# Performance work log

Hardware: AMD Instinct MI355X
Metric: run time of the kernel (lower is better)

## Reference

```python
import jax, jax.numpy as jnp
import numpy as np


def setup_inputs() -> dict:
    key = jax.random.key(0)
    ks = jax.random.split(key, 12)
    B, N, Din, D, K = 2, 1024, 64, 64, 24
    s = lambda fan_in: 1.0 / np.sqrt(fan_in)
    return {
        "feature": jax.random.normal(ks[0], (B, N, Din), jnp.float32),
        "xyz": jax.random.normal(ks[1], (B, N, 3), jnp.float32),
        "pw1": jax.random.uniform(ks[2], (Din, D), jnp.float32, -s(Din), s(Din)),
        "pb1": jax.random.uniform(ks[3], (D,), jnp.float32, -s(Din), s(Din)),
        "pw2": jax.random.uniform(ks[4], (D, D), jnp.float32, -s(D), s(D)),
        "pb2": jax.random.uniform(ks[5], (D,), jnp.float32, -s(D), s(D)),
        "rw": jax.random.uniform(ks[6], (3, D * D), jnp.float32, -s(3), s(3)),
        "rb": jax.random.uniform(ks[7], (D * D,), jnp.float32, -s(3), s(3)),
        "sw": jax.random.uniform(ks[8], (D, D), jnp.float32, -s(D), s(D)),
        "sb": jax.random.uniform(ks[9], (D,), jnp.float32, -s(D), s(D)),
        "knn_num": 24,
    }


def reference(feature, xyz, pw1, pb1, pw2, pb2, rw, rb, sw, sb, knn_num):
    B, N, _ = feature.shape
    D = pw2.shape[1]
    K = knn_num
    # KNN over xyz (squared euclidean distances, smallest K)
    sq = jnp.sum(xyz * xyz, axis=-1)  # [B,N]
    d2 = sq[:, :, None] + sq[:, None, :] - 2.0 * jnp.einsum('bnc,bmc->bnm', xyz, xyz)
    _, idx = jax.lax.top_k(-d2, K)  # [B,N,K]
    bidx = jnp.arange(B)[:, None, None]
    rel = xyz[bidx, idx] - xyz[:, :, None, :]  # [B,N,K,3]
    # prefix MLP: relu(Linear -> ReLU -> Linear)
    feat = jax.nn.relu(jax.nn.relu(feature @ pw1 + pb1) @ pw2 + pb2)  # [B,N,D]
    # per-edge weight generation + softmax over (K*D)
    w = (rel @ rw + rb).reshape(B, N, K * D, D)
    w = jax.nn.softmax(w, axis=-2)
    # gather neighbor features and aggregate
    gv = feat[bidx, idx].reshape(B, N, K * D)  # [B,N,K*D]
    out = jnp.einsum('bnm,bnmd->bnd', gv, w)  # [B,N,D]
    out = out @ sw + sb
    return (out, N)
```

## Files before the change

### kernel.cpp

```cpp
#include <hip/hip_runtime.h>
#include <math.h>

#define BB 2
#define NN 1024
#define DD 64
#define KK 24
#define NPTS (BB * NN)

#if __has_builtin(__builtin_amdgcn_exp2f)
#define EXP2(x) __builtin_amdgcn_exp2f(x)
#else
#define EXP2(x) exp2f(x)
#endif


__global__ __launch_bounds__(256) void prep_kernel(const float* __restrict__ rw,
                                                   const float* __restrict__ rb,
                                                   float* __restrict__ rwS,
                                                   float* __restrict__ rbS) {
    const float LOG2E = 1.4426950408889634f;
    int i = blockIdx.x * 256 + threadIdx.x;
    if (i < 3 * 4096) {
        rwS[i] = rw[i] * LOG2E;
    } else {
        int j = i - 3 * 4096;
        if (j < 4096) rbS[j] = rb[j] * LOG2E;
    }
}

__global__ __launch_bounds__(256) void mlp_kernel(const float* __restrict__ feature,
                                                  const float* __restrict__ pw1,
                                                  const float* __restrict__ pb1,
                                                  const float* __restrict__ pw2,
                                                  const float* __restrict__ pb2,
                                                  float* __restrict__ feat) {
    int tid = threadIdx.x;
    int r = tid >> 6;
    int d = tid & 63;
    int row = blockIdx.x * 4 + r;
    __shared__ float s_in[4][64];
    __shared__ float s_h[4][64];
    s_in[r][d] = feature[row * 64 + d];
    __syncthreads();
    float h = pb1[d];
#pragma unroll
    for (int i = 0; i < 64; i++) h = __builtin_fmaf(s_in[r][i], pw1[i * 64 + d], h);
    h = fmaxf(h, 0.f);
    s_h[r][d] = h;
    __syncthreads();
    float f = pb2[d];
#pragma unroll
    for (int i = 0; i < 64; i++) f = __builtin_fmaf(s_h[r][i], pw2[i * 64 + d], f);
    f = fmaxf(f, 0.f);
    feat[row * 64 + d] = f;
}

__global__ __launch_bounds__(64) void knn_kernel(const float* __restrict__ xyz,
                                                 int* __restrict__ idx_out) {
    int pt = blockIdx.x;
    int b = pt >> 10;
    int n = pt & 1023;
    int lane = threadIdx.x;
    const float* xb = xyz + (size_t)b * NN * 3;
    float xn = xb[n * 3 + 0], yn = xb[n * 3 + 1], zn = xb[n * 3 + 2];
    float sqn = xn * xn + yn * yn + zn * zn;
    float dist[16];
#pragma unroll
    for (int c = 0; c < 16; c++) {
        int m = c * 64 + lane;
        float xm = xb[m * 3 + 0], ym = xb[m * 3 + 1], zm = xb[m * 3 + 2];
        float sqm = xm * xm + ym * ym + zm * zm;
        float dot = xn * xm + yn * ym + zn * zm;
        dist[c] = sqn + sqm - 2.0f * dot;
    }
    for (int r = 0; r < KK; r++) {
        float best = 3.4e38f;
        int bi = 1 << 30;
#pragma unroll
        for (int c = 0; c < 16; c++) {
            if (dist[c] < best) {
                best = dist[c];
                bi = c * 64 + lane;
            }
        }
#pragma unroll
        for (int off = 32; off >= 1; off >>= 1) {
            float ob = __shfl_down(best, off);
            int oi = __shfl_down(bi, off);
            if (ob < best || (ob == best && oi < bi)) {
                best = ob;
                bi = oi;
            }
        }
        bi = __shfl(bi, 0);
        if ((bi & 63) == lane) dist[bi >> 6] = 3.4e38f;
        if (lane == 0) idx_out[pt * KK + r] = bi;
    }
}

__global__ __launch_bounds__(256) void agg_kernel(const float* __restrict__ xyz,
                                                  const float* __restrict__ feat,
                                                  const int* __restrict__ idx,
                                                  const float* __restrict__ rwS,
                                                  const float* __restrict__ rbS,
                                                  const float* __restrict__ sw,
                                                  const float* __restrict__ sb,
                                                  float* __restrict__ out) {
    int pt = blockIdx.x;
    int b = pt >> 10;
    int n = pt & 1023;
    int tid = threadIdx.x;
    int w = tid >> 6;
    int d = tid & 63;

    __shared__ float s_rel[KK][3];
    __shared__ __align__(16) float s_gvt[64][KK];
    __shared__ float s_red[8][64];
    __shared__ float s_pre[64];

    const float* xb = xyz + (size_t)b * NN * 3;
    if (tid < KK * 3) {
        int k = tid / 3, c = tid % 3;
        int nb = idx[pt * KK + k];
        s_rel[k][c] = xb[nb * 3 + c] - xb[n * 3 + c];
    }
    for (int t = tid; t < KK * 64; t += 256) {
        int k = t >> 6, j = t & 63;
        int nb = idx[pt * KK + k];
        s_gvt[j][k] = feat[((size_t)b * NN + nb) * 64 + j];
    }
    __syncthreads();

    float rx[KK], ry[KK], rz[KK];
#pragma unroll
    for (int k = 0; k < KK; k++) {
        rx[k] = s_rel[k][0];
        ry[k] = s_rel[k][1];
        rz[k] = s_rel[k][2];
    }

    float l0 = 0.f, l1 = 0.f, a0 = 0.f, a1 = 0.f;
    for (int jj = 0; jj < 16; jj++) {
        int j = w * 16 + jj;
        int col = j * 64 + d;
        float r0 = rwS[col];
        float r1 = rwS[4096 + col];
        float r2 = rwS[8192 + col];
        float rbv = rbS[col];
        float gv[KK];
        {
            const float4* gp = (const float4*)(&s_gvt[j][0]);
#pragma unroll
            for (int q = 0; q < 6; q++) {
                float4 g = gp[q];
                gv[4 * q + 0] = g.x;
                gv[4 * q + 1] = g.y;
                gv[4 * q + 2] = g.z;
                gv[4 * q + 3] = g.w;
            }
        }
#pragma unroll
        for (int k = 0; k < KK; k += 2) {
            float t0 = __builtin_fmaf(r0, rx[k], __builtin_fmaf(r1, ry[k], __builtin_fmaf(r2, rz[k], rbv)));
            float t1 = __builtin_fmaf(r0, rx[k + 1], __builtin_fmaf(r1, ry[k + 1], __builtin_fmaf(r2, rz[k + 1], rbv)));
            float e0 = EXP2(t0);
            float e1 = EXP2(t1);
            l0 += e0;
            l1 += e1;
            a0 = __builtin_fmaf(gv[k], e0, a0);
            a1 = __builtin_fmaf(gv[k + 1], e1, a1);
        }
    }
    s_red[w][d] = l0 + l1;
    s_red[4 + w][d] = a0 + a1;
    __syncthreads();
    if (tid < 64) {
        float L = s_red[0][d] + s_red[1][d] + s_red[2][d] + s_red[3][d];
        float A = s_red[4][d] + s_red[5][d] + s_red[6][d] + s_red[7][d];
        s_pre[d] = A / L;
    }
    __syncthreads();
    float part = 0.f;
#pragma unroll
    for (int dd = 0; dd < 16; dd++) {
        int drow = w * 16 + dd;
        part = __builtin_fmaf(s_pre[drow], sw[drow * 64 + d], part);
    }
    s_red[w][d] = part;
    __syncthreads();
    if (tid < 64) {
        float o = s_red[0][d] + s_red[1][d] + s_red[2][d] + s_red[3][d] + sb[d];
        out[(size_t)pt * 64 + d] = o;
    }
    if (pt == 0 && tid == 0) out[(size_t)NPTS * 64] = 1024.0f;
}

extern "C" void kernel_launch(void* const* d_in, const int* in_sizes, int n_in,
                              void* d_out, int out_size, void* d_ws, size_t ws_size,
                              hipStream_t stream) {
    const float* feature = (const float*)d_in[0];
    const float* xyz = (const float*)d_in[1];
    const float* pw1 = (const float*)d_in[2];
    const float* pb1 = (const float*)d_in[3];
    const float* pw2 = (const float*)d_in[4];
    const float* pb2 = (const float*)d_in[5];
    const float* rw = (const float*)d_in[6];
    const float* rb = (const float*)d_in[7];
    const float* sw = (const float*)d_in[8];
    const float* sb = (const float*)d_in[9];
    float* out = (float*)d_out;

    char* ws = (char*)d_ws;
    float* feat = (float*)(ws);
    int* idx = (int*)(ws + 524288);
    float* rwS = (float*)(ws + 720896);
    float* rbS = (float*)(ws + 770048);

    prep_kernel<<<(3 * 4096 + 4096 + 255) / 256, 256, 0, stream>>>(rw, rb, rwS, rbS);
    mlp_kernel<<<NPTS / 4, 256, 0, stream>>>(feature, pw1, pb1, pw2, pb2, feat);
    knn_kernel<<<NPTS, 64, 0, stream>>>(xyz, idx);
    agg_kernel<<<NPTS, 256, 0, stream>>>(xyz, feat, idx, rwS, rbS, sw, sb, out);
}
```

Baseline: 146.9 us.

## Fuse prep, MLP and KNN into one launch; pack agg math into float2 vectors

The three independent pre-kernels (weight scaling, prefix MLP, KNN) are merged into one kernel whose blocks branch on block index, cutting three launches to one. KNN now packs four points per 256-thread block instead of one per 64-thread block. In the aggregation kernel the edge-weight FMAs and accumulations use two-wide float vectors so the compiler can emit packed FP32 instructions, and the shared gather tile row stride is padded from 24 to 28 floats. Risks include branch-heavy blocks with uneven work and higher register pressure from the vector arrays.

```diff
diff --git a/kernel.cpp b/kernel.cpp
--- a/kernel.cpp
+++ b/kernel.cpp
@@ -13,91 +13,92 @@
 #define EXP2(x) exp2f(x)
 #endif
 
-
-__global__ __launch_bounds__(256) void prep_kernel(const float* __restrict__ rw,
-                                                   const float* __restrict__ rb,
-                                                   float* __restrict__ rwS,
-                                                   float* __restrict__ rbS) {
-    const float LOG2E = 1.4426950408889634f;
-    int i = blockIdx.x * 256 + threadIdx.x;
-    if (i < 3 * 4096) {
-        rwS[i] = rw[i] * LOG2E;
+typedef float v2f __attribute__((ext_vector_type(2)));
+
+
+__global__ __launch_bounds__(256) void prep_mlp_knn_kernel(
+    const float* __restrict__ feature, const float* __restrict__ xyz,
+    const float* __restrict__ pw1, const float* __restrict__ pb1,
+    const float* __restrict__ pw2, const float* __restrict__ pb2,
+    const float* __restrict__ rw, const float* __restrict__ rb,
+    float* __restrict__ feat, int* __restrict__ idx_out,
+    float* __restrict__ rwS, float* __restrict__ rbS) {
+    int bid = blockIdx.x;
+    int tid = threadIdx.x;
+
+    if (bid < 512) {
+        int r = tid >> 6;
+        int d = tid & 63;
+        int row = bid * 4 + r;
+        __shared__ float s_in[4][64];
+        __shared__ float s_h[4][64];
+        s_in[r][d] = feature[row * 64 + d];
+        __syncthreads();
+        float h = pb1[d];
+#pragma unroll
+        for (int i = 0; i < 64; i++) h = __builtin_fmaf(s_in[r][i], pw1[i * 64 + d], h);
+        h = fmaxf(h, 0.f);
+        s_h[r][d] = h;
+        __syncthreads();
+        float f = pb2[d];
+#pragma unroll
+        for (int i = 0; i < 64; i++) f = __builtin_fmaf(s_h[r][i], pw2[i * 64 + d], f);
+        f = fmaxf(f, 0.f);
+        feat[row * 64 + d] = f;
+    } else if (bid < 528) {
+        const float LOG2E = 1.4426950408889634f;
+        int t = (bid - 512) * 256 + tid;
+#pragma unroll
+        for (int q = 0; q < 4; q++) {
+            int i = t + q * 4096;
+            rwS[i] = rw[i] * LOG2E;
+        }
+        rbS[t] = rb[t] * LOG2E;
     } else {
-        int j = i - 3 * 4096;
-        if (j < 4096) rbS[j] = rb[j] * LOG2E;
+        int w = tid >> 6;
+        int lane = tid & 63;
+        int pt = (bid - 528) * 4 + w;
+        int b = pt >> 10;
+        int n = pt & 1023;
+        const float* xb = xyz + (size_t)b * NN * 3;
+        float xn = xb[n * 3 + 0], yn = xb[n * 3 + 1], zn = xb[n * 3 + 2];
+        float sqn = xn * xn + yn * yn + zn * zn;
+        float dist[16];
+#pragma unroll
+        for (int c = 0; c < 16; c++) {
+            int m = c * 64 + lane;
+            float xm = xb[m * 3 + 0], ym = xb[m * 3 + 1], zm = xb[m * 3 + 2];
+            float sqm = xm * xm + ym * ym + zm * zm;
+            float dot = xn * xm + yn * ym + zn * zm;
+            dist[c] = sqn + sqm - 2.0f * dot;
+        }
+        for (int r = 0; r < KK; r++) {
+            float best = 3.4e38f;
+            int bi = 1 << 30;
+#pragma unroll
+            for (int c = 0; c < 16; c++) {
+                if (dist[c] < best) {
+                    best = dist[c];
+                    bi = c * 64 + lane;
+                }
+            }
+#pragma unroll
+            for (int off = 32; off >= 1; off >>= 1) {
+                float ob = __shfl_down(best, off);
+                int oi = __shfl_down(bi, off);
+                if (ob < best || (ob == best && oi < bi)) {
+                    best = ob;
+                    bi = oi;
+                }
+            }
+            bi = __shfl(bi, 0);
+            if ((bi & 63) == lane) dist[bi >> 6] = 3.4e38f;
+            if (lane == 0) idx_out[pt * KK + r] = bi;
+        }
     }
 }
 
-__global__ __launch_bounds__(256) void mlp_kernel(const float* __restrict__ feature,
-                                                  const float* __restrict__ pw1,
-                                                  const float* __restrict__ pb1,
-                                                  const float* __restrict__ pw2,
-                                                  const float* __restrict__ pb2,
-                                                  float* __restrict__ feat) {
-    int tid = threadIdx.x;
-    int r = tid >> 6;
-    int d = tid & 63;
-    int row = blockIdx.x * 4 + r;
-    __shared__ float s_in[4][64];
-    __shared__ float s_h[4][64];
-    s_in[r][d] = feature[row * 64 + d];
-    __syncthreads();
-    float h = pb1[d];
-#pragma unroll
-    for (int i = 0; i < 64; i++) h = __builtin_fmaf(s_in[r][i], pw1[i * 64 + d], h);
-    h = fmaxf(h, 0.f);
-    s_h[r][d] = h;
-    __syncthreads();
-    float f = pb2[d];
-#pragma unroll
-    for (int i = 0; i < 64; i++) f = __builtin_fmaf(s_h[r][i], pw2[i * 64 + d], f);
-    f = fmaxf(f, 0.f);
-    feat[row * 64 + d] = f;
-}
-
-__global__ __launch_bounds__(64) void knn_kernel(const float* __restrict__ xyz,
-                                                 int* __restrict__ idx_out) {
-    int pt = blockIdx.x;
-    int b = pt >> 10;
-    int n = pt & 1023;
-    int lane = threadIdx.x;
-    const float* xb = xyz + (size_t)b * NN * 3;
-    float xn = xb[n * 3 + 0], yn = xb[n * 3 + 1], zn = xb[n * 3 + 2];
-    float sqn = xn * xn + yn * yn + zn * zn;
-    float dist[16];
-#pragma unroll
-    for (int c = 0; c < 16; c++) {
-        int m = c * 64 + lane;
-        float xm = xb[m * 3 + 0], ym = xb[m * 3 + 1], zm = xb[m * 3 + 2];
-        float sqm = xm * xm + ym * ym + zm * zm;
-        float dot = xn * xm + yn * ym + zn * zm;
-        dist[c] = sqn + sqm - 2.0f * dot;
-    }
-    for (int r = 0; r < KK; r++) {
-        float best = 3.4e38f;
-        int bi = 1 << 30;
-#pragma unroll
-        for (int c = 0; c < 16; c++) {
-            if (dist[c] < best) {
-                best = dist[c];
-                bi = c * 64 + lane;
-            }
-        }
-#pragma unroll
-        for (int off = 32; off >= 1; off >>= 1) {
-            float ob = __shfl_down(best, off);
-            int oi = __shfl_down(bi, off);
-            if (ob < best || (ob == best && oi < bi)) {
-                best = ob;
-                bi = oi;
-            }
-        }
-        bi = __shfl(bi, 0);
-        if ((bi & 63) == lane) dist[bi >> 6] = 3.4e38f;
-        if (lane == 0) idx_out[pt * KK + r] = bi;
-    }
-}
-
+#define GVS 28
 __global__ __launch_bounds__(256) void agg_kernel(const float* __restrict__ xyz,
                                                   const float* __restrict__ feat,
                                                   const int* __restrict__ idx,
@@ -114,7 +115,7 @@
     int d = tid & 63;
 
     __shared__ float s_rel[KK][3];
-    __shared__ __align__(16) float s_gvt[64][KK];
+    __shared__ __align__(16) float s_gvt[64][GVS];
     __shared__ float s_red[8][64];
     __shared__ float s_pre[64];
 
@@ -131,15 +132,15 @@
     }
     __syncthreads();
 
-    float rx[KK], ry[KK], rz[KK];
-#pragma unroll
-    for (int k = 0; k < KK; k++) {
-        rx[k] = s_rel[k][0];
-        ry[k] = s_rel[k][1];
-        rz[k] = s_rel[k][2];
-    }
-
-    float l0 = 0.f, l1 = 0.f, a0 = 0.f, a1 = 0.f;
+    v2f rx[12], ry[12], rz[12];
+#pragma unroll
+    for (int k = 0; k < 12; k++) {
+        rx[k] = (v2f){s_rel[2 * k][0], s_rel[2 * k + 1][0]};
+        ry[k] = (v2f){s_rel[2 * k][1], s_rel[2 * k + 1][1]};
+        rz[k] = (v2f){s_rel[2 * k][2], s_rel[2 * k + 1][2]};
+    }
+
+    v2f l0 = {0.f, 0.f}, l1 = {0.f, 0.f}, a0 = {0.f, 0.f}, a1 = {0.f, 0.f};
     for (int jj = 0; jj < 16; jj++) {
         int j = w * 16 + jj;
         int col = j * 64 + d;
@@ -147,32 +148,25 @@
         float r1 = rwS[4096 + col];
         float r2 = rwS[8192 + col];
         float rbv = rbS[col];
-        float gv[KK];
-        {
-            const float4* gp = (const float4*)(&s_gvt[j][0]);
-#pragma unroll
-            for (int q = 0; q < 6; q++) {
-                float4 g = gp[q];
-                gv[4 * q + 0] = g.x;
-                gv[4 * q + 1] = g.y;
-                gv[4 * q + 2] = g.z;
-                gv[4 * q + 3] = g.w;
-            }
-        }
-#pragma unroll
-        for (int k = 0; k < KK; k += 2) {
-            float t0 = __builtin_fmaf(r0, rx[k], __builtin_fmaf(r1, ry[k], __builtin_fmaf(r2, rz[k], rbv)));
-            float t1 = __builtin_fmaf(r0, rx[k + 1], __builtin_fmaf(r1, ry[k + 1], __builtin_fmaf(r2, rz[k + 1], rbv)));
-            float e0 = EXP2(t0);
-            float e1 = EXP2(t1);
+        v2f R0 = {r0, r0}, R1 = {r1, r1}, R2 = {r2, r2}, RB = {rbv, rbv};
+        const float4* g4 = (const float4*)(&s_gvt[j][0]);
+#pragma unroll
+        for (int q = 0; q < 6; q++) {
+            float4 g = g4[q];
+            v2f ga = {g.x, g.y};
+            v2f gb = {g.z, g.w};
+            v2f t0 = rx[2 * q] * R0 + (ry[2 * q] * R1 + (rz[2 * q] * R2 + RB));
+            v2f t1 = rx[2 * q + 1] * R0 + (ry[2 * q + 1] * R1 + (rz[2 * q + 1] * R2 + RB));
+            v2f e0 = {EXP2(t0.x), EXP2(t0.y)};
+            v2f e1 = {EXP2(t1.x), EXP2(t1.y)};
             l0 += e0;
             l1 += e1;
-            a0 = __builtin_fmaf(gv[k], e0, a0);
-            a1 = __builtin_fmaf(gv[k + 1], e1, a1);
-        }
-    }
-    s_red[w][d] = l0 + l1;
-    s_red[4 + w][d] = a0 + a1;
+            a0 += ga * e0;
+            a1 += gb * e1;
+        }
+    }
+    s_red[w][d] = l0.x + l0.y + l1.x + l1.y;
+    s_red[4 + w][d] = a0.x + a0.y + a1.x + a1.y;
     __syncthreads();
     if (tid < 64) {
         float L = s_red[0][d] + s_red[1][d] + s_red[2][d] + s_red[3][d];
@@ -216,8 +210,7 @@
     float* rwS = (float*)(ws + 720896);
     float* rbS = (float*)(ws + 770048);
 
-    prep_kernel<<<(3 * 4096 + 4096 + 255) / 256, 256, 0, stream>>>(rw, rb, rwS, rbS);
-    mlp_kernel<<<NPTS / 4, 256, 0, stream>>>(feature, pw1, pb1, pw2, pb2, feat);
-    knn_kernel<<<NPTS, 64, 0, stream>>>(xyz, idx);
+    prep_mlp_knn_kernel<<<1040, 256, 0, stream>>>(feature, xyz, pw1, pb1, pw2, pb2,
+                                                  rw, rb, feat, idx, rwS, rbS);
     agg_kernel<<<NPTS, 256, 0, stream>>>(xyz, feat, idx, rwS, rbS, sw, sb, out);
 }
```

Measured after the change: 139.2 us. 1.06x faster.
